# Performance work log

Hardware: AMD Instinct MI355X
Metric: run time of the kernel (lower is better)

The kernel has to match this reference:

```python
import jax, jax.numpy as jnp
import numpy as np

PADDING = 1

def setup_inputs() -> dict:
    key = jax.random.key(0)
    k1, k2 = jax.random.split(key)
    imgs = jax.random.normal(k1, (8, 32, 32, 32), dtype=jnp.float32)
    kernel = jax.random.normal(k2, (32, 32, 3, 3), dtype=jnp.float32)
    return {"imgs": imgs, "kernel": kernel}

def reference(imgs, kernel):
    # Tropical max-plus 'convolution' (kind='conv': kernel spatially flipped),
    # groups=1, stride=1, dilation=1, padding=PADDING with semifield zero = -inf.
    B, C, H, W = imgs.shape
    O, Ck, kh, kw = kernel.shape
    OY = H + 2 * PADDING - (kh - 1)
    OX = W + 2 * PADDING - (kw - 1)
    neg_inf = jnp.array(-jnp.inf, dtype=imgs.dtype)
    x = jnp.pad(imgs, ((0, 0), (0, 0), (PADDING, PADDING), (PADDING, PADDING)),
                constant_values=neg_inf)
    # conv flips the kernel spatially
    k = kernel[:, :, ::-1, ::-1]
    # im2col windows: [B, C, kh*kw, OY, OX] (small fixed loop over kernel taps)
    windows = jnp.stack(
        [x[:, :, dy:dy + OY, dx:dx + OX] for dy in range(kh) for dx in range(kw)],
        axis=2,
    )
    # broadcast 'multiply' (tropical: add): [B, O, C, kh*kw, OY, OX]
    mult = windows[:, None] + k.reshape(1, O, C, kh * kw, 1, 1)
    # tropical add-reduce (max) over channels and kernel taps
    out = jnp.max(mult, axis=(2, 3))  # [B, O, OY, OX]
    return out
```

## Files before the change

kernel.cpp:

```cpp
#include <hip/hip_runtime.h>
#include <math.h>


constexpr int B = 8, C = 32, O = 32, H = 32, W = 32;
constexpr int HW = H * W;

typedef float f4 __attribute__((ext_vector_type(4)));

__device__ __forceinline__ float f3(float a, float b, float c) {
  return fmaxf(fmaxf(a, b), c);
}

__device__ __forceinline__ f4 ld4u(const float* p) {
  f4 q;
  __builtin_memcpy(&q, p, sizeof(q));
  return q;
}

__global__ __launch_bounds__(256, 2) void trop_conv_kernel(
    const float* __restrict__ img, const float* __restrict__ kern,
    float* __restrict__ out) {
  const int tid = threadIdx.x;
  const int blk = blockIdx.x;
  const int yh = blk & 1;
  const int o = (blk >> 1) & 31;
  const int b = blk >> 6;

  const int seg = tid & 15;
  const int x0 = seg * 2;
  const int r = tid >> 4;
  const int y = yh * 16 + r;

  int xb = x0 - 1;
  xb = xb < 0 ? 0 : xb;
  xb = xb > 28 ? 28 : xb;
  int ym = y - 1; ym = ym < 0 ? 0 : ym;
  int yp = y + 1; yp = yp > 31 ? 31 : yp;
  const int off0 = ym * W + xb;
  const int off1 = y * W + xb;
  const int off2 = yp * W + xb;

  const bool top = (y == 0);
  const bool bot = (y == 31);
  const bool xz = (x0 == 0);
  const bool xe = (x0 == 30);
  const float NEG = -__builtin_huge_valf();

  const float* ib = img + b * C * HW;
  const float* kc = kern + o * 288;

  float acc0 = NEG, acc1 = NEG;

#pragma unroll 4
  for (int c = 0; c < C; ++c) {
    const float* ic = ib + c * HW;
    const float* kp = kc + c * 9;
    const float w0 = kp[0], w1 = kp[1], w2 = kp[2], w3 = kp[3], w4 = kp[4],
                w5 = kp[5], w6 = kp[6], w7 = kp[7], w8 = kp[8];

    const f4 q0 = ld4u(ic + off0);
    const f4 q1 = ld4u(ic + off1);
    const f4 q2 = ld4u(ic + off2);

    const float am = xz ? NEG : (xe ? q0.y : q0.x);
    const float a0 = xe ? q0.z : (xz ? q0.x : q0.y);
    const float a1 = xe ? q0.w : (xz ? q0.y : q0.z);
    const float a2 = xe ? NEG : (xz ? q0.z : q0.w);

    const float bm = xz ? NEG : (xe ? q1.y : q1.x);
    const float b0 = xe ? q1.z : (xz ? q1.x : q1.y);
    const float b1 = xe ? q1.w : (xz ? q1.y : q1.z);
    const float b2 = xe ? NEG : (xz ? q1.z : q1.w);

    const float cm = xz ? NEG : (xe ? q2.y : q2.x);
    const float c0 = xe ? q2.z : (xz ? q2.x : q2.y);
    const float c1 = xe ? q2.w : (xz ? q2.y : q2.z);
    const float c2 = xe ? NEG : (xz ? q2.z : q2.w);

    float t0a = f3(am + w8, a0 + w7, a1 + w6);
    float t1a = f3(a0 + w8, a1 + w7, a2 + w6);
    t0a = top ? NEG : t0a;
    t1a = top ? NEG : t1a;

    const float t0b = f3(bm + w5, b0 + w4, b1 + w3);
    const float t1b = f3(b0 + w5, b1 + w4, b2 + w3);

    float t0c = f3(cm + w2, c0 + w1, c1 + w0);
    float t1c = f3(c0 + w2, c1 + w1, c2 + w0);
    t0c = bot ? NEG : t0c;
    t1c = bot ? NEG : t1c;

    acc0 = fmaxf(acc0, f3(t0a, t0b, t0c));
    acc1 = fmaxf(acc1, f3(t1a, t1b, t1c));
  }

  float2 res = make_float2(acc0, acc1);
  *reinterpret_cast<float2*>(&out[((b * O + o) * H + y) * W + x0]) = res;
}

extern "C" void kernel_launch(void* const* d_in, const int* in_sizes, int n_in,
                              void* d_out, int out_size, void* d_ws, size_t ws_size,
                              hipStream_t stream) {
  const float* img = (const float*)d_in[0];
  const float* kern = (const float*)d_in[1];
  float* out = (float*)d_out;
  trop_conv_kernel<<<dim3(512), dim3(256), 0, stream>>>(img, kern, out);
}
```

Before: 63.58 us.

## Split channel reduction across thread groups with shared-memory max combine

Each block now covers 8 output rows with 512 threads split into four channel groups of 8 channels. Partial max accumulators are combined through shared memory before a single group writes the output. This quadruples thread-level parallelism and shortens each thread's serial loop to hide load latency. The cost is a block barrier, a shared-memory reduction, and idle threads during the final combine.

```diff
diff --git a/kernel.cpp b/kernel.cpp
--- a/kernel.cpp
+++ b/kernel.cpp
@@ -17,19 +17,24 @@
   return q;
 }
 
-__global__ __launch_bounds__(256, 2) void trop_conv_kernel(
+__global__ __launch_bounds__(512, 8) void trop_conv_kernel(
     const float* __restrict__ img, const float* __restrict__ kern,
     float* __restrict__ out) {
+  __shared__ float red[3 * 128 * 2];
+
   const int tid = threadIdx.x;
   const int blk = blockIdx.x;
-  const int yh = blk & 1;
-  const int o = (blk >> 1) & 31;
-  const int b = blk >> 6;
+  const int yq = blk & 3;
+  const int o = (blk >> 2) & 31;
+  const int b = blk >> 7;
 
-  const int seg = tid & 15;
+  const int lid = tid & 127;
+  const int cg = __builtin_amdgcn_readfirstlane(tid >> 7);
+
+  const int seg = lid & 15;
   const int x0 = seg * 2;
-  const int r = tid >> 4;
-  const int y = yh * 16 + r;
+  const int r = lid >> 4;
+  const int y = yq * 8 + r;
 
   int xb = x0 - 1;
   xb = xb < 0 ? 0 : xb;
@@ -46,15 +51,15 @@
   const bool xe = (x0 == 30);
   const float NEG = -__builtin_huge_valf();
 
-  const float* ib = img + b * C * HW;
-  const float* kc = kern + o * 288;
+  const float* icb = img + b * C * HW + cg * 8 * HW;
+  const float* kc = kern + o * 288 + cg * 8 * 9;
 
   float acc0 = NEG, acc1 = NEG;
 
-#pragma unroll 4
-  for (int c = 0; c < C; ++c) {
-    const float* ic = ib + c * HW;
-    const float* kp = kc + c * 9;
+#pragma unroll 2
+  for (int i = 0; i < 8; ++i) {
+    const float* ic = icb + i * HW;
+    const float* kp = kc + i * 9;
     const float w0 = kp[0], w1 = kp[1], w2 = kp[2], w3 = kp[3], w4 = kp[4],
                 w5 = kp[5], w6 = kp[6], w7 = kp[7], w8 = kp[8];
 
@@ -94,8 +99,19 @@
     acc1 = fmaxf(acc1, f3(t1a, t1b, t1c));
   }
 
-  float2 res = make_float2(acc0, acc1);
-  *reinterpret_cast<float2*>(&out[((b * O + o) * H + y) * W + x0]) = res;
+  if (cg > 0) {
+    red[(cg - 1) * 256 + lid * 2] = acc0;
+    red[(cg - 1) * 256 + lid * 2 + 1] = acc1;
+  }
+  __syncthreads();
+  if (cg == 0) {
+    acc0 = fmaxf(fmaxf(acc0, red[lid * 2]),
+                 fmaxf(red[256 + lid * 2], red[512 + lid * 2]));
+    acc1 = fmaxf(fmaxf(acc1, red[lid * 2 + 1]),
+                 fmaxf(red[256 + lid * 2 + 1], red[512 + lid * 2 + 1]));
+    float2 res = make_float2(acc0, acc1);
+    *reinterpret_cast<float2*>(&out[((b * O + o) * H + y) * W + x0]) = res;
+  }
 }
 
 extern "C" void kernel_launch(void* const* d_in, const int* in_sizes, int n_in,
@@ -104,5 +120,5 @@
   const float* img = (const float*)d_in[0];
   const float* kern = (const float*)d_in[1];
   float* out = (float*)d_out;
-  trop_conv_kernel<<<dim3(512), dim3(256), 0, stream>>>(img, kern, out);
+  trop_conv_kernel<<<dim3(1024), dim3(512), 0, stream>>>(img, kern, out);
 }
```

After: 62.67 us. Within noise of the previous version (-1.4%).
